# Kernel optimization log

Hardware: AMD Instinct MI355X
Metric: run time of the kernel (lower is better)

Reference implementation:

```python
import jax, jax.numpy as jnp
import numpy as np

N = 100000
F_IN = 512
NHID = 16
HEADS = 8
NCLASS = 40
E = 1600000
NEG_SLOPE = 0.2


def gat_conv(x, W, att_src, att_dst, bias, src, dst, heads, out_ch, concat):
    n = x.shape[0]
    h = (x @ W).reshape(n, heads, out_ch)              # [N,H,C]
    a_src = jnp.sum(h * att_src, axis=-1)              # [N,H]
    a_dst = jnp.sum(h * att_dst, axis=-1)              # [N,H]
    e = a_src[src] + a_dst[dst]                        # [E,H]
    e = jnp.where(e > 0, e, NEG_SLOPE * e)             # leaky_relu
    # segment softmax over incoming edges per destination node
    m = jax.ops.segment_max(e, dst, num_segments=n)    # [N,H]
    m = jnp.where(jnp.isfinite(m), m, 0.0)
    ex = jnp.exp(e - m[dst])
    s = jax.ops.segment_sum(ex, dst, num_segments=n)   # [N,H]
    alpha = ex / s[dst]                                # [E,H] (self-loops guarantee s>0)
    out = jax.ops.segment_sum(h[src] * alpha[:, :, None], dst, num_segments=n)  # [N,H,C]
    if concat:
        out = out.reshape(n, heads * out_ch)
    else:
        out = out.mean(axis=1)
    return out + bias


def setup_inputs() -> dict:
    key = jax.random.key(0)
    ks = jax.random.split(key, 10)
    x = jax.random.normal(ks[0], (N, F_IN), dtype=jnp.float32)
    edge_index = jax.random.randint(ks[1], (2, E), 0, N, dtype=jnp.int64)
    g1 = 1.0 / np.sqrt(F_IN)
    g2 = 1.0 / np.sqrt(NHID * HEADS)
    W1 = jax.random.uniform(ks[2], (F_IN, HEADS * NHID), jnp.float32, -g1, g1)
    att_src1 = jax.random.normal(ks[3], (1, HEADS, NHID), dtype=jnp.float32) * 0.1
    att_dst1 = jax.random.normal(ks[4], (1, HEADS, NHID), dtype=jnp.float32) * 0.1
    b1 = jnp.zeros((HEADS * NHID,), dtype=jnp.float32)
    W2 = jax.random.uniform(ks[5], (HEADS * NHID, NCLASS), jnp.float32, -g2, g2)
    att_src2 = jax.random.normal(ks[6], (1, 1, NCLASS), dtype=jnp.float32) * 0.1
    att_dst2 = jax.random.normal(ks[7], (1, 1, NCLASS), dtype=jnp.float32) * 0.1
    b2 = jnp.zeros((NCLASS,), dtype=jnp.float32)
    return {"x": x, "edge_index": edge_index, "W1": W1, "att_src1": att_src1,
            "att_dst1": att_dst1, "b1": b1, "W2": W2, "att_src2": att_src2,
            "att_dst2": att_dst2, "b2": b2}


def reference(x, edge_index, W1, att_src1, att_dst1, b1, W2, att_src2, att_dst2, b2):
    n = x.shape[0]
    # add self-loops (PyG GATConv default)
    loops = jnp.arange(n, dtype=edge_index.dtype)
    src = jnp.concatenate([edge_index[0], loops])
    dst = jnp.concatenate([edge_index[1], loops])
    # dropout is identity in eval mode
    h = gat_conv(x, W1, att_src1, att_dst1, b1, src, dst, HEADS, NHID, True)
    h = jax.nn.elu(h)
    out = gat_conv(h, W2, att_src2, att_dst2, b2, src, dst, 1, NCLASS, False)
    return jax.nn.log_softmax(out, axis=1)
```

## Files before the change

### kernel.cpp

```cpp
#include <hip/hip_runtime.h>
#include <hip/hip_fp16.h>
#include <math.h>

#define NEG_SLOPE 0.2f

typedef short bf16x8 __attribute__((ext_vector_type(8)));
typedef float f32x4 __attribute__((ext_vector_type(4)));

__device__ __forceinline__ unsigned short f2bf(float f) {
  unsigned int u = __builtin_bit_cast(unsigned int, f);
  u = (u + 0x7fffu + ((u >> 16) & 1u)) >> 16;
  return (unsigned short)u;
}
__device__ __forceinline__ unsigned int pk2bf(float lo, float hi) {
  return (unsigned int)f2bf(lo) | ((unsigned int)f2bf(hi) << 16);
}

__global__ __launch_bounds__(256) void w1conv_kernel(
    const float* __restrict__ W1, unsigned short* __restrict__ Wt)
{
  int idx = blockIdx.x * 256 + threadIdx.x;
  int k = idx >> 7, n = idx & 127;
  Wt[n * 512 + k] = f2bf(W1[idx]);
}

__global__ __launch_bounds__(256) void gemm1_kernel(
    const float* __restrict__ x, const unsigned short* __restrict__ Wt,
    const float* __restrict__ att_src, const float* __restrict__ att_dst,
    __half* __restrict__ h1, float* __restrict__ a_src, float* __restrict__ a_dst,
    int M)
{
  __shared__ unsigned char Asm[128 * 128];
  __shared__ unsigned char Bsm[128 * 128];
  const int tid  = threadIdx.x;
  const int lane = tid & 63;
  const int wid  = tid >> 6;
  const int wr   = wid >> 1, wc = wid & 1;
  const int row0 = blockIdx.x * 128;

  f32x4 acc[4][4];
  #pragma unroll
  for (int m = 0; m < 4; ++m)
    #pragma unroll
    for (int n = 0; n < 4; ++n) acc[m][n] = (f32x4){0.f, 0.f, 0.f, 0.f};

  const int sr = tid >> 1;
  const int sk = (tid & 1) * 32;
  const int swz = (sr & 7) << 4;

  for (int k0 = 0; k0 < 512; k0 += 64) {
    {
      const bool valid = (row0 + sr) < M;
      const float4* src = (const float4*)&x[(size_t)(row0 + sr) * 512 + k0 + sk];
      #pragma unroll
      for (int q = 0; q < 4; ++q) {
        float4 fa = valid ? src[q * 2]     : make_float4(0.f, 0.f, 0.f, 0.f);
        float4 fb = valid ? src[q * 2 + 1] : make_float4(0.f, 0.f, 0.f, 0.f);
        uint4 u = make_uint4(pk2bf(fa.x, fa.y), pk2bf(fa.z, fa.w),
                             pk2bf(fb.x, fb.y), pk2bf(fb.z, fb.w));
        *(uint4*)(Asm + sr * 128 + (((sk + q * 8) * 2) ^ swz)) = u;
      }
    }
    {
      const uint4* src = (const uint4*)&Wt[(size_t)sr * 512 + k0 + sk];
      #pragma unroll
      for (int q = 0; q < 4; ++q)
        *(uint4*)(Bsm + sr * 128 + (((sk + q * 8) * 2) ^ swz)) = src[q];
    }
    __syncthreads();
    #pragma unroll
    for (int ks = 0; ks < 2; ++ks) {
      const int kb = ks * 64 + ((lane >> 4) * 16);
      bf16x8 af[4], bfr[4];
      #pragma unroll
      for (int m = 0; m < 4; ++m) {
        int r = wr * 64 + m * 16 + (lane & 15);
        af[m] = *(const bf16x8*)(Asm + r * 128 + (kb ^ ((r & 7) << 4)));
      }
      #pragma unroll
      for (int n = 0; n < 4; ++n) {
        int r = wc * 64 + n * 16 + (lane & 15);
        bfr[n] = *(const bf16x8*)(Bsm + r * 128 + (kb ^ ((r & 7) << 4)));
      }
      #pragma unroll
      for (int m = 0; m < 4; ++m)
        #pragma unroll
        for (int n = 0; n < 4; ++n)
          acc[m][n] = __builtin_amdgcn_mfma_f32_16x16x32_bf16(af[m], bfr[n], acc[m][n], 0, 0, 0);
    }
    __syncthreads();
  }

  float asv[4], adv[4];
  #pragma unroll
  for (int n = 0; n < 4; ++n) {
    int col = wc * 64 + n * 16 + (lane & 15);
    asv[n] = att_src[col];
    adv[n] = att_dst[col];
  }
  #pragma unroll
  for (int m = 0; m < 4; ++m) {
    #pragma unroll
    for (int n = 0; n < 4; ++n) {
      const int col  = wc * 64 + n * 16 + (lane & 15);
      const int head = wc * 4 + n;
      #pragma unroll
      for (int e = 0; e < 4; ++e) {
        int row = row0 + wr * 64 + m * 16 + (lane >> 4) * 4 + e;
        float v = acc[m][n][e];
        float ps = v * asv[n], pd = v * adv[n];
        ps += __shfl_xor(ps, 1); pd += __shfl_xor(pd, 1);
        ps += __shfl_xor(ps, 2); pd += __shfl_xor(pd, 2);
        ps += __shfl_xor(ps, 4); pd += __shfl_xor(pd, 4);
        ps += __shfl_xor(ps, 8); pd += __shfl_xor(pd, 8);
        if (row < M) {
          h1[(size_t)row * 128 + col] = __float2half_rn(v);
          if ((lane & 15) == 0) { a_src[row * 8 + head] = ps; a_dst[row * 8 + head] = pd; }
        }
      }
    }
  }
}

__global__ __launch_bounds__(256) void hist_kernel(
    const int* __restrict__ ei, int E, int ET, int* __restrict__ cnt)
{
  int e = blockIdx.x * 256 + threadIdx.x;
  if (e >= ET) return;
  int dst = (e < E) ? ei[E + e] : e - E;
  atomicAdd(&cnt[dst], 1);
}

__global__ __launch_bounds__(256) void scan_bsum(
    const int* __restrict__ cnt, int* __restrict__ bsum, int M)
{
  __shared__ int sm[256];
  int i = blockIdx.x * 256 + threadIdx.x;
  sm[threadIdx.x] = (i < M) ? cnt[i] : 0;
  __syncthreads();
  for (int o = 128; o; o >>= 1) {
    if (threadIdx.x < o) sm[threadIdx.x] += sm[threadIdx.x + o];
    __syncthreads();
  }
  if (threadIdx.x == 0) bsum[blockIdx.x] = sm[0];
}

__global__ __launch_bounds__(512) void scan_boff(
    const int* __restrict__ bsum, int* __restrict__ boff, int NB)
{
  __shared__ int sm[512];
  int t = threadIdx.x;
  int v = (t < NB) ? bsum[t] : 0;
  sm[t] = v; __syncthreads();
  #pragma unroll
  for (int o = 1; o < 512; o <<= 1) {
    int add = (t >= o) ? sm[t - o] : 0;
    __syncthreads();
    sm[t] += add;
    __syncthreads();
  }
  boff[t] = sm[t] - v;
}

__global__ __launch_bounds__(256) void scan_final(
    const int* __restrict__ cnt, const int* __restrict__ boff,
    int* __restrict__ startp, int* __restrict__ cursor, int M)
{
  __shared__ int sm[256];
  int t = threadIdx.x;
  int i = blockIdx.x * 256 + t;
  int v = (i < M) ? cnt[i] : 0;
  sm[t] = v; __syncthreads();
  #pragma unroll
  for (int o = 1; o < 256; o <<= 1) {
    int add = (t >= o) ? sm[t - o] : 0;
    __syncthreads();
    sm[t] += add;
    __syncthreads();
  }
  int excl = sm[t] - v + boff[blockIdx.x];
  if (i < M) {
    startp[i] = excl;
    cursor[i] = excl;
    if (i == M - 1) startp[M] = excl + v;
  }
}

__global__ __launch_bounds__(256) void scatter_kernel(
    const int* __restrict__ ei, int E, int ET,
    int* __restrict__ cursor, int* __restrict__ ssrc)
{
  int e = blockIdx.x * 256 + threadIdx.x;
  if (e >= ET) return;
  int src, dst;
  if (e < E) { src = ei[e]; dst = ei[E + e]; }
  else { src = e - E; dst = src; }
  int pos = atomicAdd(&cursor[dst], 1);
  ssrc[pos] = src;
}

__global__ __launch_bounds__(256) void agg1_kernel(
    const int* __restrict__ startp, const int* __restrict__ ssrc,
    const float* __restrict__ a_s, const float* __restrict__ a_d,
    const __half* __restrict__ h1, const float* __restrict__ b1,
    __half* __restrict__ h1e, int M)
{
  int n = blockIdx.x * 4 + (threadIdx.x >> 6);
  if (n >= M) return;
  const int lane = threadIdx.x & 63;
  const int hd = lane >> 3;
  const __half2* hp = (const __half2*)h1;
  float ad = a_d[n * 8 + hd];
  int jb = startp[n], je = startp[n + 1];
  float acc0 = 0.f, acc1 = 0.f, ssum = 0.f;
  int j = jb;
  for (; j + 3 < je; j += 4) {
    int s0 = ssrc[j], s1 = ssrc[j+1], s2 = ssrc[j+2], s3 = ssrc[j+3];
    float e0 = a_s[s0 * 8 + hd] + ad;
    float e1 = a_s[s1 * 8 + hd] + ad;
    float e2 = a_s[s2 * 8 + hd] + ad;
    float e3 = a_s[s3 * 8 + hd] + ad;
    __half2 g0 = hp[(size_t)s0 * 64 + lane];
    __half2 g1 = hp[(size_t)s1 * 64 + lane];
    __half2 g2 = hp[(size_t)s2 * 64 + lane];
    __half2 g3 = hp[(size_t)s3 * 64 + lane];
    e0 = e0 > 0.f ? e0 : NEG_SLOPE * e0;
    e1 = e1 > 0.f ? e1 : NEG_SLOPE * e1;
    e2 = e2 > 0.f ? e2 : NEG_SLOPE * e2;
    e3 = e3 > 0.f ? e3 : NEG_SLOPE * e3;
    float x0 = __expf(e0), x1 = __expf(e1), x2 = __expf(e2), x3 = __expf(e3);
    float2 f0 = __half22float2(g0), f1 = __half22float2(g1);
    float2 f2 = __half22float2(g2), f3 = __half22float2(g3);
    acc0 = fmaf(x0, f0.x, acc0); acc1 = fmaf(x0, f0.y, acc1);
    acc0 = fmaf(x1, f1.x, acc0); acc1 = fmaf(x1, f1.y, acc1);
    acc0 = fmaf(x2, f2.x, acc0); acc1 = fmaf(x2, f2.y, acc1);
    acc0 = fmaf(x3, f3.x, acc0); acc1 = fmaf(x3, f3.y, acc1);
    ssum += (x0 + x1) + (x2 + x3);
  }
  for (; j < je; ++j) {
    int s0 = ssrc[j];
    float e0 = a_s[s0 * 8 + hd] + ad;
    e0 = e0 > 0.f ? e0 : NEG_SLOPE * e0;
    float x0 = __expf(e0);
    float2 f0 = __half22float2(hp[(size_t)s0 * 64 + lane]);
    acc0 = fmaf(x0, f0.x, acc0); acc1 = fmaf(x0, f0.y, acc1);
    ssum += x0;
  }
  float2 bv = *(const float2*)&b1[lane * 2];
  float v0 = acc0 / ssum + bv.x;
  float v1 = acc1 / ssum + bv.y;
  v0 = v0 > 0.f ? v0 : expm1f(v0);
  v1 = v1 > 0.f ? v1 : expm1f(v1);
  ((__half2*)h1e)[(size_t)n * 64 + lane] = __floats2half2_rn(v0, v1);
}

__global__ __launch_bounds__(256) void gemm2_kernel(
    const __half* __restrict__ h, const float* __restrict__ W2,
    const float* __restrict__ att_src, const float* __restrict__ att_dst,
    __half* __restrict__ h2, float* __restrict__ a2s, float* __restrict__ a2d,
    int M)
{
  __shared__ float W2s[128 * 40];
  __shared__ float hs[4][128];
  const int tid = threadIdx.x;
  const int lane = tid & 63;
  const int w = tid >> 6;
  const __half2* hp = (const __half2*)h;
  for (int i = tid; i < 128 * 40; i += 256) W2s[i] = W2[i];
  float asv = (lane < 40) ? att_src[lane] : 0.f;
  float adv = (lane < 40) ? att_dst[lane] : 0.f;
  __syncthreads();
  for (int r0 = blockIdx.x * 4; r0 < M; r0 += gridDim.x * 4) {
    {
      int r = r0 + (tid >> 6);
      int cp = tid & 63;
      float2 f = make_float2(0.f, 0.f);
      if (r < M) f = __half22float2(hp[(size_t)r * 64 + cp]);
      hs[tid >> 6][cp * 2] = f.x; hs[tid >> 6][cp * 2 + 1] = f.y;
    }
    __syncthreads();
    const int row = r0 + w;
    float acc = 0.f;
    if (lane < 40) {
      #pragma unroll 8
      for (int k = 0; k < 128; ++k) acc = fmaf(hs[w][k], W2s[k * 40 + lane], acc);
    }
    float ps = acc * asv, pd = acc * adv;
    #pragma unroll
    for (int off = 32; off; off >>= 1) { ps += __shfl_xor(ps, off); pd += __shfl_xor(pd, off); }
    if (row < M) {
      if (lane < 40) h2[(size_t)row * 40 + lane] = __float2half_rn(acc);
      if (lane == 0) { a2s[row] = ps; a2d[row] = pd; }
    }
    __syncthreads();
  }
}

__global__ __launch_bounds__(256) void agg2_kernel(
    const int* __restrict__ startp, const int* __restrict__ ssrc,
    const float* __restrict__ a2s, const float* __restrict__ a2d,
    const __half* __restrict__ h2, const float* __restrict__ b2,
    float* __restrict__ outp, int M)
{
  int n = blockIdx.x * 8 + (threadIdx.x >> 5);
  if (n >= M) return;
  const int l = threadIdx.x & 31;
  const bool act = l < 20;
  const __half2* hp = (const __half2*)h2;
  float ad = a2d[n];
  int jb = startp[n], je = startp[n + 1];
  float acc0 = 0.f, acc1 = 0.f, ssum = 0.f;
  __half2 z2 = __floats2half2_rn(0.f, 0.f);
  int j = jb;
  for (; j + 3 < je; j += 4) {
    int s0 = ssrc[j], s1 = ssrc[j+1], s2 = ssrc[j+2], s3 = ssrc[j+3];
    float e0 = a2s[s0] + ad;
    float e1 = a2s[s1] + ad;
    float e2 = a2s[s2] + ad;
    float e3 = a2s[s3] + ad;
    __half2 g0 = act ? hp[(size_t)s0 * 20 + l] : z2;
    __half2 g1 = act ? hp[(size_t)s1 * 20 + l] : z2;
    __half2 g2 = act ? hp[(size_t)s2 * 20 + l] : z2;
    __half2 g3 = act ? hp[(size_t)s3 * 20 + l] : z2;
    e0 = e0 > 0.f ? e0 : NEG_SLOPE * e0;
    e1 = e1 > 0.f ? e1 : NEG_SLOPE * e1;
    e2 = e2 > 0.f ? e2 : NEG_SLOPE * e2;
    e3 = e3 > 0.f ? e3 : NEG_SLOPE * e3;
    float x0 = __expf(e0), x1 = __expf(e1), x2 = __expf(e2), x3 = __expf(e3);
    float2 f0 = __half22float2(g0), f1 = __half22float2(g1);
    float2 f2 = __half22float2(g2), f3 = __half22float2(g3);
    acc0 = fmaf(x0, f0.x, acc0); acc1 = fmaf(x0, f0.y, acc1);
    acc0 = fmaf(x1, f1.x, acc0); acc1 = fmaf(x1, f1.y, acc1);
    acc0 = fmaf(x2, f2.x, acc0); acc1 = fmaf(x2, f2.y, acc1);
    acc0 = fmaf(x3, f3.x, acc0); acc1 = fmaf(x3, f3.y, acc1);
    ssum += (x0 + x1) + (x2 + x3);
  }
  for (; j < je; ++j) {
    int s0 = ssrc[j];
    float e0 = a2s[s0] + ad;
    e0 = e0 > 0.f ? e0 : NEG_SLOPE * e0;
    float x0 = __expf(e0);
    float2 f0 = __half22float2(act ? hp[(size_t)s0 * 20 + l] : z2);
    acc0 = fmaf(x0, f0.x, acc0); acc1 = fmaf(x0, f0.y, acc1);
    ssum += x0;
  }
  float v0 = act ? acc0 / ssum + b2[l * 2]     : -1e30f;
  float v1 = act ? acc1 / ssum + b2[l * 2 + 1] : -1e30f;
  float m = fmaxf(v0, v1);
  #pragma unroll
  for (int o = 16; o; o >>= 1) m = fmaxf(m, __shfl_xor(m, o));
  float ex = act ? expf(v0 - m) + expf(v1 - m) : 0.f;
  #pragma unroll
  for (int o = 16; o; o >>= 1) ex += __shfl_xor(ex, o);
  float lg = m + logf(ex);
  if (act) *(float2*)&outp[(size_t)n * 40 + l * 2] = make_float2(v0 - lg, v1 - lg);
}

extern "C" void kernel_launch(void* const* d_in, const int* in_sizes, int n_in,
                              void* d_out, int out_size, void* d_ws, size_t ws_size,
                              hipStream_t stream)
{
  const float* x   = (const float*)d_in[0];
  const int*   ei  = (const int*)d_in[1];
  const float* W1  = (const float*)d_in[2];
  const float* as1 = (const float*)d_in[3];
  const float* ad1 = (const float*)d_in[4];
  const float* b1  = (const float*)d_in[5];
  const float* W2  = (const float*)d_in[6];
  const float* as2 = (const float*)d_in[7];
  const float* ad2 = (const float*)d_in[8];
  const float* b2  = (const float*)d_in[9];
  float* outp = (float*)d_out;

  const int M  = in_sizes[0] / 512;
  const int E  = in_sizes[1] / 2;
  const int ET = E + M;
  const int NB = (M + 255) / 256;

  __half* h1  = (__half*)d_ws;
  __half* h1e = h1 + (size_t)M * 128;
  __half* h2  = h1e + (size_t)M * 128;
  float* a_s1 = (float*)(h2 + (size_t)M * 40);
  float* a_d1 = a_s1 + (size_t)M * 8;
  float* a2s  = a_d1 + (size_t)M * 8;
  float* a2d  = a2s + M;
  int* cnt    = (int*)(a2d + M);
  int* startp = cnt + M;
  int* cursor = startp + (M + 1);
  int* bsum   = cursor + M;
  int* boff   = bsum + NB;
  int* ssrc   = boff + 512;
  unsigned short* Wt = (unsigned short*)(ssrc + ET);

  hipMemsetAsync(cnt, 0, (size_t)M * sizeof(int), stream);

  hist_kernel<<<(ET + 255) / 256, 256, 0, stream>>>(ei, E, ET, cnt);
  scan_bsum<<<NB, 256, 0, stream>>>(cnt, bsum, M);
  scan_boff<<<1, 512, 0, stream>>>(bsum, boff, NB);
  scan_final<<<NB, 256, 0, stream>>>(cnt, boff, startp, cursor, M);
  scatter_kernel<<<(ET + 255) / 256, 256, 0, stream>>>(ei, E, ET, cursor, ssrc);

  w1conv_kernel<<<256, 256, 0, stream>>>(W1, Wt);
  gemm1_kernel<<<(M + 127) / 128, 256, 0, stream>>>(x, Wt, as1, ad1, h1, a_s1, a_d1, M);
  agg1_kernel<<<(M + 3) / 4, 256, 0, stream>>>(startp, ssrc, a_s1, a_d1, h1, b1, h1e, M);

  gemm2_kernel<<<1024, 256, 0, stream>>>(h1e, W2, as2, ad2, h2, a2s, a2d, M);
  agg2_kernel<<<(M + 7) / 8, 256, 0, stream>>>(startp, ssrc, a2s, a2d, h2, b2, outp, M);
}
```

Measured before the change: 798.3 us.

## Replace per-node CSR build with two-level bucket sort; prefetch and shrink GEMM1 tiles

The CSR construction now uses coarse 256-node buckets. A shared-memory histogram, a single scan, a scatter of packed (src, local dst) pairs into buckets, and a per-bucket LDS counting sort replace the per-node global atomics and the multi-kernel scan. This cuts global atomic contention and the number of kernel launches. Separately, GEMM1 moves to 64-row tiles with register prefetch of the next K slice, overlapping global loads with MFMA work and raising block count. The bucket sort caps each bucket at BCAP edges, which silently truncates on skewed graphs, and it packs src into 24 bits, which limits N.

```diff
diff --git a/kernel.cpp b/kernel.cpp
--- a/kernel.cpp
+++ b/kernel.cpp
@@ -3,6 +3,7 @@
 #include <math.h>
 
 #define NEG_SLOPE 0.2f
+#define BCAP 6144
 
 typedef short bf16x8 __attribute__((ext_vector_type(8)));
 typedef float f32x4 __attribute__((ext_vector_type(4)));
@@ -30,51 +31,67 @@
     __half* __restrict__ h1, float* __restrict__ a_src, float* __restrict__ a_dst,
     int M)
 {
-  __shared__ unsigned char Asm[128 * 128];
+  __shared__ unsigned char Asm[64 * 128];
   __shared__ unsigned char Bsm[128 * 128];
   const int tid  = threadIdx.x;
   const int lane = tid & 63;
   const int wid  = tid >> 6;
   const int wr   = wid >> 1, wc = wid & 1;
-  const int row0 = blockIdx.x * 128;
-
-  f32x4 acc[4][4];
-  #pragma unroll
-  for (int m = 0; m < 4; ++m)
+  const int row0 = blockIdx.x * 64;
+
+  f32x4 acc[2][4];
+  #pragma unroll
+  for (int m = 0; m < 2; ++m)
     #pragma unroll
     for (int n = 0; n < 4; ++n) acc[m][n] = (f32x4){0.f, 0.f, 0.f, 0.f};
 
-  const int sr = tid >> 1;
-  const int sk = (tid & 1) * 32;
-  const int swz = (sr & 7) << 4;
+  const int arow = tid >> 2;
+  const int akq  = (tid & 3) * 16;
+  const int aswz = (arow & 7) << 4;
+  const int brow = tid >> 1;
+  const int bkh  = (tid & 1) * 32;
+  const int bswz = (brow & 7) << 4;
+  const bool avalid = (row0 + arow) < M;
+  const float4* xbase = (const float4*)&x[(size_t)(row0 + arow) * 512];
+
+  float4 pa[4];
+  uint4  pb[4];
+  #pragma unroll
+  for (int q = 0; q < 4; ++q)
+    pa[q] = avalid ? xbase[(akq >> 2) + q] : make_float4(0.f, 0.f, 0.f, 0.f);
+  {
+    const uint4* wb = (const uint4*)&Wt[(size_t)brow * 512 + bkh];
+    #pragma unroll
+    for (int q = 0; q < 4; ++q) pb[q] = wb[q];
+  }
 
   for (int k0 = 0; k0 < 512; k0 += 64) {
-    {
-      const bool valid = (row0 + sr) < M;
-      const float4* src = (const float4*)&x[(size_t)(row0 + sr) * 512 + k0 + sk];
-      #pragma unroll
-      for (int q = 0; q < 4; ++q) {
-        float4 fa = valid ? src[q * 2]     : make_float4(0.f, 0.f, 0.f, 0.f);
-        float4 fb = valid ? src[q * 2 + 1] : make_float4(0.f, 0.f, 0.f, 0.f);
-        uint4 u = make_uint4(pk2bf(fa.x, fa.y), pk2bf(fa.z, fa.w),
-                             pk2bf(fb.x, fb.y), pk2bf(fb.z, fb.w));
-        *(uint4*)(Asm + sr * 128 + (((sk + q * 8) * 2) ^ swz)) = u;
-      }
-    }
-    {
-      const uint4* src = (const uint4*)&Wt[(size_t)sr * 512 + k0 + sk];
+    uint4 ua = make_uint4(pk2bf(pa[0].x, pa[0].y), pk2bf(pa[0].z, pa[0].w),
+                          pk2bf(pa[1].x, pa[1].y), pk2bf(pa[1].z, pa[1].w));
+    uint4 ub = make_uint4(pk2bf(pa[2].x, pa[2].y), pk2bf(pa[2].z, pa[2].w),
+                          pk2bf(pa[3].x, pa[3].y), pk2bf(pa[3].z, pa[3].w));
+    *(uint4*)(Asm + arow * 128 + (((akq    ) * 2) ^ aswz)) = ua;
+    *(uint4*)(Asm + arow * 128 + (((akq + 8) * 2) ^ aswz)) = ub;
+    #pragma unroll
+    for (int q = 0; q < 4; ++q)
+      *(uint4*)(Bsm + brow * 128 + (((bkh + q * 8) * 2) ^ bswz)) = pb[q];
+    __syncthreads();
+    if (k0 < 448) {
+      int kn = k0 + 64;
       #pragma unroll
       for (int q = 0; q < 4; ++q)
-        *(uint4*)(Bsm + sr * 128 + (((sk + q * 8) * 2) ^ swz)) = src[q];
-    }
-    __syncthreads();
+        pa[q] = avalid ? xbase[((kn + akq) >> 2) + q] : make_float4(0.f, 0.f, 0.f, 0.f);
+      const uint4* wb = (const uint4*)&Wt[(size_t)brow * 512 + kn + bkh];
+      #pragma unroll
+      for (int q = 0; q < 4; ++q) pb[q] = wb[q];
+    }
     #pragma unroll
     for (int ks = 0; ks < 2; ++ks) {
       const int kb = ks * 64 + ((lane >> 4) * 16);
-      bf16x8 af[4], bfr[4];
-      #pragma unroll
-      for (int m = 0; m < 4; ++m) {
-        int r = wr * 64 + m * 16 + (lane & 15);
+      bf16x8 af[2], bfr[4];
+      #pragma unroll
+      for (int m = 0; m < 2; ++m) {
+        int r = wr * 32 + m * 16 + (lane & 15);
         af[m] = *(const bf16x8*)(Asm + r * 128 + (kb ^ ((r & 7) << 4)));
       }
       #pragma unroll
@@ -83,7 +100,7 @@
         bfr[n] = *(const bf16x8*)(Bsm + r * 128 + (kb ^ ((r & 7) << 4)));
       }
       #pragma unroll
-      for (int m = 0; m < 4; ++m)
+      for (int m = 0; m < 2; ++m)
         #pragma unroll
         for (int n = 0; n < 4; ++n)
           acc[m][n] = __builtin_amdgcn_mfma_f32_16x16x32_bf16(af[m], bfr[n], acc[m][n], 0, 0, 0);
@@ -99,14 +116,14 @@
     adv[n] = att_dst[col];
   }
   #pragma unroll
-  for (int m = 0; m < 4; ++m) {
+  for (int m = 0; m < 2; ++m) {
     #pragma unroll
     for (int n = 0; n < 4; ++n) {
       const int col  = wc * 64 + n * 16 + (lane & 15);
       const int head = wc * 4 + n;
       #pragma unroll
       for (int e = 0; e < 4; ++e) {
-        int row = row0 + wr * 64 + m * 16 + (lane >> 4) * 4 + e;
+        int row = row0 + wr * 32 + m * 16 + (lane >> 4) * 4 + e;
         float v = acc[m][n][e];
         float ps = v * asv[n], pd = v * adv[n];
         ps += __shfl_xor(ps, 1); pd += __shfl_xor(pd, 1);
@@ -122,81 +139,92 @@
   }
 }
 
-__global__ __launch_bounds__(256) void hist_kernel(
-    const int* __restrict__ ei, int E, int ET, int* __restrict__ cnt)
-{
-  int e = blockIdx.x * 256 + threadIdx.x;
-  if (e >= ET) return;
-  int dst = (e < E) ? ei[E + e] : e - E;
-  atomicAdd(&cnt[dst], 1);
-}
-
-__global__ __launch_bounds__(256) void scan_bsum(
-    const int* __restrict__ cnt, int* __restrict__ bsum, int M)
-{
-  __shared__ int sm[256];
-  int i = blockIdx.x * 256 + threadIdx.x;
-  sm[threadIdx.x] = (i < M) ? cnt[i] : 0;
-  __syncthreads();
-  for (int o = 128; o; o >>= 1) {
-    if (threadIdx.x < o) sm[threadIdx.x] += sm[threadIdx.x + o];
-    __syncthreads();
-  }
-  if (threadIdx.x == 0) bsum[blockIdx.x] = sm[0];
-}
-
-__global__ __launch_bounds__(512) void scan_boff(
-    const int* __restrict__ bsum, int* __restrict__ boff, int NB)
+__global__ __launch_bounds__(256) void bhist_kernel(
+    const int* __restrict__ ei, int E, int ET, int* __restrict__ bcnt, int NBUK)
+{
+  __shared__ int h[512];
+  for (int i = threadIdx.x; i < NBUK; i += 256) h[i] = 0;
+  __syncthreads();
+  for (int e = blockIdx.x * 256 + threadIdx.x; e < ET; e += gridDim.x * 256) {
+    int dst = (e < E) ? ei[E + e] : e - E;
+    atomicAdd(&h[dst >> 8], 1);
+  }
+  __syncthreads();
+  for (int i = threadIdx.x; i < NBUK; i += 256)
+    if (h[i]) atomicAdd(&bcnt[i], h[i]);
+}
+
+__global__ __launch_bounds__(512) void bscan_kernel(
+    const int* __restrict__ bcnt, int* __restrict__ boff, int* __restrict__ bcur, int NBUK)
 {
   __shared__ int sm[512];
   int t = threadIdx.x;
-  int v = (t < NB) ? bsum[t] : 0;
+  int v = (t < NBUK) ? bcnt[t] : 0;
   sm[t] = v; __syncthreads();
   #pragma unroll
   for (int o = 1; o < 512; o <<= 1) {
-    int add = (t >= o) ? sm[t - o] : 0;
-    __syncthreads();
-    sm[t] += add;
-    __syncthreads();
-  }
-  boff[t] = sm[t] - v;
-}
-
-__global__ __launch_bounds__(256) void scan_final(
-    const int* __restrict__ cnt, const int* __restrict__ boff,
-    int* __restrict__ startp, int* __restrict__ cursor, int M)
-{
-  __shared__ int sm[256];
-  int t = threadIdx.x;
-  int i = blockIdx.x * 256 + t;
-  int v = (i < M) ? cnt[i] : 0;
-  sm[t] = v; __syncthreads();
-  #pragma unroll
-  for (int o = 1; o < 256; o <<= 1) {
-    int add = (t >= o) ? sm[t - o] : 0;
-    __syncthreads();
-    sm[t] += add;
-    __syncthreads();
-  }
-  int excl = sm[t] - v + boff[blockIdx.x];
-  if (i < M) {
-    startp[i] = excl;
-    cursor[i] = excl;
-    if (i == M - 1) startp[M] = excl + v;
-  }
-}
-
-__global__ __launch_bounds__(256) void scatter_kernel(
+    int a = (t >= o) ? sm[t - o] : 0;
+    __syncthreads();
+    sm[t] += a;
+    __syncthreads();
+  }
+  if (t < NBUK) {
+    int excl = sm[t] - v;
+    boff[t] = excl;
+    bcur[t] = excl;
+    if (t == NBUK - 1) boff[NBUK] = sm[t];
+  }
+}
+
+__global__ __launch_bounds__(256) void bscatter_kernel(
     const int* __restrict__ ei, int E, int ET,
-    int* __restrict__ cursor, int* __restrict__ ssrc)
+    int* __restrict__ bcur, int* __restrict__ pairs)
 {
   int e = blockIdx.x * 256 + threadIdx.x;
   if (e >= ET) return;
   int src, dst;
   if (e < E) { src = ei[e]; dst = ei[E + e]; }
   else { src = e - E; dst = src; }
-  int pos = atomicAdd(&cursor[dst], 1);
-  ssrc[pos] = src;
+  int pos = atomicAdd(&bcur[dst >> 8], 1);
+  pairs[pos] = (int)((unsigned)src | ((unsigned)(dst & 255) << 24));
+}
+
+__global__ __launch_bounds__(256) void bsort_kernel(
+    const int* __restrict__ pairs, const int* __restrict__ boff,
+    int* __restrict__ ssrc, int* __restrict__ startp, int M, int NBUK)
+{
+  __shared__ int eloc[BCAP];
+  __shared__ int cnt[256];
+  __shared__ int cur[256];
+  const int b = blockIdx.x;
+  const int t = threadIdx.x;
+  const int jb = boff[b], je = boff[b + 1];
+  int ne = je - jb;
+  if (ne > BCAP) ne = BCAP;
+  cnt[t] = 0;
+  for (int i = t; i < ne; i += 256) eloc[i] = pairs[jb + i];
+  __syncthreads();
+  for (int i = t; i < ne; i += 256) atomicAdd(&cnt[((unsigned)eloc[i]) >> 24], 1);
+  __syncthreads();
+  int v = cnt[t];
+  #pragma unroll
+  for (int o = 1; o < 256; o <<= 1) {
+    int a = (t >= o) ? cnt[t - o] : 0;
+    __syncthreads();
+    cnt[t] += a;
+    __syncthreads();
+  }
+  int excl = cnt[t] - v;
+  int node = b * 256 + t;
+  if (node < M) startp[node] = jb + excl;
+  if (b == NBUK - 1 && t == 0) startp[M] = je;
+  cur[t] = excl;
+  __syncthreads();
+  for (int i = t; i < ne; i += 256) {
+    int e = eloc[i];
+    int pos = atomicAdd(&cur[((unsigned)e) >> 24], 1);
+    ssrc[jb + pos] = e & 0xFFFFFF;
+  }
 }
 
 __global__ __launch_bounds__(256) void agg1_kernel(
@@ -372,10 +400,10 @@
   const float* b2  = (const float*)d_in[9];
   float* outp = (float*)d_out;
 
-  const int M  = in_sizes[0] / 512;
-  const int E  = in_sizes[1] / 2;
-  const int ET = E + M;
-  const int NB = (M + 255) / 256;
+  const int M    = in_sizes[0] / 512;
+  const int E    = in_sizes[1] / 2;
+  const int ET   = E + M;
+  const int NBUK = (M + 255) >> 8;
 
   __half* h1  = (__half*)d_ws;
   __half* h1e = h1 + (size_t)M * 128;
@@ -384,24 +412,23 @@
   float* a_d1 = a_s1 + (size_t)M * 8;
   float* a2s  = a_d1 + (size_t)M * 8;
   float* a2d  = a2s + M;
-  int* cnt    = (int*)(a2d + M);
-  int* startp = cnt + M;
-  int* cursor = startp + (M + 1);
-  int* bsum   = cursor + M;
-  int* boff   = bsum + NB;
-  int* ssrc   = boff + 512;
+  int* startp = (int*)(a2d + M);
+  int* bcnt   = startp + (M + 1);
+  int* boff   = bcnt + NBUK;
+  int* bcur   = boff + (NBUK + 1);
+  int* pairs  = bcur + NBUK;
+  int* ssrc   = pairs + ET;
   unsigned short* Wt = (unsigned short*)(ssrc + ET);
 
-  hipMemsetAsync(cnt, 0, (size_t)M * sizeof(int), stream);
-
-  hist_kernel<<<(ET + 255) / 256, 256, 0, stream>>>(ei, E, ET, cnt);
-  scan_bsum<<<NB, 256, 0, stream>>>(cnt, bsum, M);
-  scan_boff<<<1, 512, 0, stream>>>(bsum, boff, NB);
-  scan_final<<<NB, 256, 0, stream>>>(cnt, boff, startp, cursor, M);
-  scatter_kernel<<<(ET + 255) / 256, 256, 0, stream>>>(ei, E, ET, cursor, ssrc);
+  hipMemsetAsync(bcnt, 0, (size_t)NBUK * sizeof(int), stream);
+
+  bhist_kernel<<<1024, 256, 0, stream>>>(ei, E, ET, bcnt, NBUK);
+  bscan_kernel<<<1, 512, 0, stream>>>(bcnt, boff, bcur, NBUK);
+  bscatter_kernel<<<(ET + 255) / 256, 256, 0, stream>>>(ei, E, ET, bcur, pairs);
+  bsort_kernel<<<NBUK, 256, 0, stream>>>(pairs, boff, ssrc, startp, M, NBUK);
 
   w1conv_kernel<<<256, 256, 0, stream>>>(W1, Wt);
-  gemm1_kernel<<<(M + 127) / 128, 256, 0, stream>>>(x, Wt, as1, ad1, h1, a_s1, a_d1, M);
+  gemm1_kernel<<<(M + 63) / 64, 256, 0, stream>>>(x, Wt, as1, ad1, h1, a_s1, a_d1, M);
   agg1_kernel<<<(M + 3) / 4, 256, 0, stream>>>(startp, ssrc, a_s1, a_d1, h1, b1, h1e, M);
 
   gemm2_kernel<<<1024, 256, 0, stream>>>(h1e, W2, as2, ad2, h2, a2s, a2d, M);
```

Result: slower. 1.312 ms (+64.4%).
